# Performance work log

Measured on AMD Instinct MI355X. Metric: run time of the kernel, lower is better.

Reference implementation:

```python
import jax, jax.numpy as jnp
import numpy as np

EPS = 1e-6

def setup_inputs() -> dict:
    key = jax.random.key(0)
    k1, k2, k3, k4, k5 = jax.random.split(key, 5)
    B, Lq, Lk, D, Dc = 8, 1024, 8192, 256, 128
    q = jax.random.normal(k1, (B, Lq, D), dtype=jnp.float32)
    k_q = jax.random.randint(k2, (B, Lk, Dc), 0, 16, dtype=jnp.int32)  # 4-bit codes
    k_scale = jax.random.uniform(k3, (B, 1, Dc), dtype=jnp.float32)
    k_zero = jax.random.uniform(k4, (B, 1, Dc), dtype=jnp.float32) * 15.0
    W_up = jax.random.normal(k5, (D, Dc), dtype=jnp.float32) / np.sqrt(Dc)
    return {"q": q, "k_q": k_q, "k_scale": k_scale, "k_zero": k_zero, "W_up": W_up}

def reference(q, k_q, k_scale, k_zero, W_up):
    # int4 dequantization: (B, Lk, Dc)
    k_c = k_scale * (k_q.astype(jnp.float32) - k_zero)
    # low-rank decompress (nn.Linear(d_compressed, d_model, bias=False)): k = k_c @ W_up.T -> (B, Lk, D)
    k = jnp.einsum('blc,dc->bld', k_c, W_up)
    # squared norms (raw values used in diff, clamped values used in denominator)
    q_sq = jnp.sum(q * q, axis=-1)  # (B, Lq)
    k_sq = jnp.sum(k * k, axis=-1)  # (B, Lk)
    q_norm_sq = jnp.minimum(q_sq, 1.0 - EPS)
    k_norm_sq = jnp.minimum(k_sq, 1.0 - EPS)
    # ||q_i - k_j||^2 via expansion (same math as materializing the diff tensor)
    qk = jnp.einsum('bqd,bkd->bqk', q, k)  # (B, Lq, Lk)
    diff_norm_sq = jnp.maximum(q_sq[:, :, None] + k_sq[:, None, :] - 2.0 * qk, 0.0)
    denom = (1.0 - q_norm_sq)[:, :, None] * (1.0 - k_norm_sq)[:, None, :] + EPS
    dist = jnp.arccosh(1.0 + 2.0 * diff_norm_sq / denom)  # (B, Lq, Lk)
    return dist
```

## Files before the change

kernel.cpp:

```cpp
#include <hip/hip_runtime.h>
#include <hip/hip_bf16.h>

#define B_   8
#define LQ   1024
#define LK   8192
#define D_   256
#define DC   128
#define EPSF 1e-6f

typedef __attribute__((ext_vector_type(8))) short short8;
typedef __attribute__((ext_vector_type(4))) float floatx4;

static __device__ __forceinline__ floatx4 mfma16(short8 a, short8 b, floatx4 c) {
    return __builtin_amdgcn_mfma_f32_16x16x32_bf16(a, b, c, 0, 0, 0);
}
static __device__ __forceinline__ float fast_rcp(float x)  { return __builtin_amdgcn_rcpf(x); }
static __device__ __forceinline__ float fast_sqrt(float x) { return __builtin_amdgcn_sqrtf(x); }
static __device__ __forceinline__ float fast_ln(float x)   { return 0.69314718056f * __builtin_amdgcn_logf(x); }

static __device__ __forceinline__ void gl16(const void* g, void* l) {
    __builtin_amdgcn_global_load_lds(
        (const __attribute__((address_space(1))) unsigned int*)g,
        (__attribute__((address_space(3))) unsigned int*)l, 16, 0, 0);
}

__global__ __launch_bounds__(512) void k_G(const float* __restrict__ W,
                                           __hip_bfloat16* __restrict__ G,
                                           __hip_bfloat16* __restrict__ Wt) {
    __shared__ float red[512];
    int c1 = blockIdx.x;
    int t = threadIdx.x, c2 = t & 127, h = t >> 7;
    int d0 = h * 64;
    float a0 = 0.f, a1 = 0.f, a2 = 0.f, a3 = 0.f;
#pragma unroll 4
    for (int d = 0; d < 64; d += 4) {
        a0 += W[(size_t)(d0 + d + 0) * DC + c1] * W[(size_t)(d0 + d + 0) * DC + c2];
        a1 += W[(size_t)(d0 + d + 1) * DC + c1] * W[(size_t)(d0 + d + 1) * DC + c2];
        a2 += W[(size_t)(d0 + d + 2) * DC + c1] * W[(size_t)(d0 + d + 2) * DC + c2];
        a3 += W[(size_t)(d0 + d + 3) * DC + c1] * W[(size_t)(d0 + d + 3) * DC + c2];
    }
    red[t] = (a0 + a1) + (a2 + a3);
    if (t < 256) Wt[(size_t)c1 * D_ + t] = __float2bfloat16(W[(size_t)t * DC + c1]);
    __syncthreads();
    if (h == 0)
        G[c1 * DC + c2] =
            __float2bfloat16(red[c2] + red[128 + c2] + red[256 + c2] + red[384 + c2]);
}

__global__ __launch_bounds__(256) void k_qproj(const float* __restrict__ q,
                                               const __hip_bfloat16* __restrict__ Wt,
                                               __hip_bfloat16* __restrict__ qproj,
                                               float* __restrict__ q_sq) {
    __shared__ __hip_bfloat16 sA[32 * 72];
    __shared__ __hip_bfloat16 sB[128 * 72];
    int t = threadIdx.x, lane = t & 63, w = t >> 6;
    int quad = lane >> 4, li = lane & 15;
    int wm = w >> 1, wn = w & 1;
    int row0 = blockIdx.x * 32;

    float psum[2] = {0.f, 0.f};
    floatx4 acc[4];
#pragma unroll
    for (int nt = 0; nt < 4; ++nt) acc[nt] = (floatx4){0.f, 0.f, 0.f, 0.f};

    for (int kc4 = 0; kc4 < 4; ++kc4) {
#pragma unroll
        for (int it = 0; it < 2; ++it) {
            int idx = it * 256 + t;
            int r = idx >> 4, pos = idx & 15;
            float4 v = *(const float4*)(q + (size_t)(row0 + r) * D_ + kc4 * 64 + pos * 4);
            psum[it] += v.x * v.x + v.y * v.y + v.z * v.z + v.w * v.w;
            __hip_bfloat16* dst = &sA[r * 72 + pos * 4];
            dst[0] = __float2bfloat16(v.x); dst[1] = __float2bfloat16(v.y);
            dst[2] = __float2bfloat16(v.z); dst[3] = __float2bfloat16(v.w);
        }
#pragma unroll
        for (int it = 0; it < 4; ++it) {
            int e = it * 256 + t;
            int c = e >> 3, ch = e & 7;
            *(uint4*)&sB[c * 72 + ch * 8] =
                *(const uint4*)(Wt + (size_t)c * D_ + kc4 * 64 + ch * 8);
        }
        __syncthreads();
        short8 af[2];
#pragma unroll
        for (int ks = 0; ks < 2; ++ks)
            af[ks] = *(const short8*)&sA[(wm * 16 + li) * 72 + ks * 32 + quad * 8];
#pragma unroll
        for (int nt = 0; nt < 4; ++nt)
#pragma unroll
            for (int ks = 0; ks < 2; ++ks) {
                short8 bf = *(const short8*)&sB[((wn * 4 + nt) * 16 + li) * 72 + ks * 32 + quad * 8];
                acc[nt] = mfma16(af[ks], bf, acc[nt]);
            }
        __syncthreads();
    }
#pragma unroll
    for (int nt = 0; nt < 4; ++nt)
#pragma unroll
        for (int r = 0; r < 4; ++r) {
            int row = wm * 16 + quad * 4 + r;
            qproj[(size_t)(row0 + row) * DC + (wn * 4 + nt) * 16 + li] =
                __float2bfloat16(acc[nt][r]);
        }
#pragma unroll
    for (int it = 0; it < 2; ++it) {
        float s = psum[it];
        s += __shfl_xor(s, 1); s += __shfl_xor(s, 2);
        s += __shfl_xor(s, 4); s += __shfl_xor(s, 8);
        if (li == 0) q_sq[row0 + it * 16 + w * 4 + quad] = s;
    }
}

__global__ __launch_bounds__(256) void k_dq_ksq(const int* __restrict__ kq,
                                                const float* __restrict__ kscale,
                                                const float* __restrict__ kzero,
                                                const __hip_bfloat16* __restrict__ G,
                                                __hip_bfloat16* __restrict__ kc,
                                                float* __restrict__ k_sq) {
    __shared__ __hip_bfloat16 sK[64 * 132];
    int t = threadIdx.x, lane = t & 63, w = t >> 6;
    int quad = lane >> 4, li = lane & 15;
    int b = blockIdx.x >> 7, l0 = (blockIdx.x & 127) * 64;

    const int4* codes = (const int4*)(kq + ((size_t)b * LK + l0) * DC);
    int col = (t & 31) * 4;
    float4 sc = *(const float4*)(kscale + b * DC + col);
    float4 zp = *(const float4*)(kzero + b * DC + col);
    __hip_bfloat16* kco = kc + ((size_t)b * LK + l0) * DC;
#pragma unroll
    for (int it = 0; it < 8; ++it) {
        int idx = it * 256 + t;
        int r = idx >> 5;
        int4 c4 = codes[idx];
        __hip_bfloat16 tmp[4];
        tmp[0] = __float2bfloat16(sc.x * ((float)c4.x - zp.x));
        tmp[1] = __float2bfloat16(sc.y * ((float)c4.y - zp.y));
        tmp[2] = __float2bfloat16(sc.z * ((float)c4.z - zp.z));
        tmp[3] = __float2bfloat16(sc.w * ((float)c4.w - zp.w));
        *(uint2*)&sK[r * 132 + col] = *(const uint2*)tmp;
        *(uint2*)(kco + idx * 4)    = *(const uint2*)tmp;
    }
    __syncthreads();

    short8 af[4];
#pragma unroll
    for (int ks = 0; ks < 4; ++ks)
        af[ks] = *(const short8*)&sK[(w * 16 + li) * 132 + ks * 32 + quad * 8];
    float s4[4] = {0.f, 0.f, 0.f, 0.f};
#pragma unroll
    for (int nt = 0; nt < 8; ++nt) {
        floatx4 a0 = (floatx4){0.f, 0.f, 0.f, 0.f};
#pragma unroll
        for (int ks = 0; ks < 4; ++ks) {
            short8 bf = *(const short8*)(G + (size_t)(nt * 16 + li) * DC + ks * 32 + quad * 8);
            a0 = mfma16(af[ks], bf, a0);
        }
        int c2 = nt * 16 + li;
#pragma unroll
        for (int r = 0; r < 4; ++r)
            s4[r] += a0[r] * __bfloat162float(sK[(w * 16 + quad * 4 + r) * 132 + c2]);
    }
#pragma unroll
    for (int r = 0; r < 4; ++r) {
        float v = s4[r];
        v += __shfl_xor(v, 1); v += __shfl_xor(v, 2);
        v += __shfl_xor(v, 4); v += __shfl_xor(v, 8);
        if (li == 0)
            k_sq[(size_t)b * LK + l0 + w * 16 + quad * 4 + r] = v;
    }
}

__global__ __launch_bounds__(256, 4) void k_main(const __hip_bfloat16* __restrict__ qproj,
                                                 const __hip_bfloat16* __restrict__ kc,
                                                 const float* __restrict__ q_sq,
                                                 const float* __restrict__ k_sq,
                                                 float* __restrict__ out) {
    __shared__ __hip_bfloat16 sA[128 * 64];
    __shared__ __hip_bfloat16 sB[128 * 64];
    int t = threadIdx.x, lane = t & 63, w = t >> 6;
    int quad = lane >> 4, li = lane & 15;
    int wm = w >> 1, wn = w & 1;
    int bid = blockIdx.x;
    int b   = bid & 7;
    int rem = bid >> 3;
    int m0  = (rem & 7) << 7;
    int n0  = (rem >> 3) << 7;
    const char* Ag = (const char*)(qproj + ((size_t)b * LQ + m0) * DC);
    const char* Bg = (const char*)(kc   + ((size_t)b * LK + n0) * DC);

    int lrow = lane >> 3;
    int lch  = (lane & 7) ^ lrow;

    floatx4 acc[4][4];
#pragma unroll
    for (int i = 0; i < 4; ++i)
#pragma unroll
        for (int j = 0; j < 4; ++j)
            acc[i][j] = (floatx4){0.f, 0.f, 0.f, 0.f};

#pragma unroll
    for (int h = 0; h < 2; ++h) {
#pragma unroll
        for (int it = 0; it < 4; ++it) {
            int rbase = it * 32 + w * 8;
            size_t goff = (size_t)(rbase + lrow) * 256 + (size_t)(h * 8 + lch) * 16;
            gl16(Ag + goff, (char*)sA + rbase * 128);
            gl16(Bg + goff, (char*)sB + rbase * 128);
        }
        __syncthreads();
#pragma unroll
        for (int ks = 0; ks < 2; ++ks) {
            int ac = ((ks * 4 + quad) ^ (li & 7)) * 16;
            short8 qf[4], kf[4];
#pragma unroll
            for (int i = 0; i < 4; ++i) {
                qf[i] = *(const short8*)((const char*)sA + (wm * 64 + i * 16 + li) * 128 + ac);
                kf[i] = *(const short8*)((const char*)sB + (wn * 64 + i * 16 + li) * 128 + ac);
            }
#pragma unroll
            for (int i = 0; i < 4; ++i)
#pragma unroll
                for (int j = 0; j < 4; ++j)
                    acc[i][j] = mfma16(kf[j], qf[i], acc[i][j]);
        }
        if (h == 0) __syncthreads();
    }

    floatx4 ks4[4], kn4[4];
#pragma unroll
    for (int j = 0; j < 4; ++j) {
        ks4[j] = *(const floatx4*)(k_sq + (size_t)b * LK + n0 + wn * 64 + j * 16 + quad * 4);
#pragma unroll
        for (int r = 0; r < 4; ++r)
            kn4[j][r] = 1.f - fminf(ks4[j][r], 1.f - EPSF);
    }
#pragma unroll
    for (int i = 0; i < 4; ++i) {
        int m = m0 + wm * 64 + i * 16 + li;
        float qs  = q_sq[(size_t)b * LQ + m];
        float omq = 1.f - fminf(qs, 1.f - EPSF);
        float* orow = out + ((size_t)b * LQ + m) * (size_t)LK + n0 + wn * 64;
#pragma unroll
        for (int j = 0; j < 4; ++j) {
            floatx4 o;
#pragma unroll
            for (int r = 0; r < 4; ++r) {
                float diff  = fmaxf(qs + ks4[j][r] - 2.f * acc[i][j][r], 0.f);
                float delta = 2.f * diff * fast_rcp(omq * kn4[j][r] + EPSF);
                float sq    = fast_sqrt(delta * (delta + 2.f));
                o[r] = fast_ln(1.f + delta + sq);
            }
            __builtin_nontemporal_store(o, (floatx4*)(orow + j * 16 + quad * 4));
        }
    }
}

extern "C" void kernel_launch(void* const* d_in, const int* in_sizes, int n_in,
                              void* d_out, int out_size, void* d_ws, size_t ws_size,
                              hipStream_t stream) {
    const float* q      = (const float*)d_in[0];
    const int*   kq     = (const int*)d_in[1];
    const float* kscale = (const float*)d_in[2];
    const float* kzero  = (const float*)d_in[3];
    const float* W      = (const float*)d_in[4];
    float* out = (float*)d_out;

    char* ws = (char*)d_ws;
    __hip_bfloat16* qproj = (__hip_bfloat16*)(ws);
    __hip_bfloat16* kc    = (__hip_bfloat16*)(ws + 2097152);
    __hip_bfloat16* G     = (__hip_bfloat16*)(ws + 18874368);
    float*          q_sq  = (float*)(ws + 18907136);
    float*          k_sq  = (float*)(ws + 18939904);
    __hip_bfloat16* Wt    = kc;

    k_G     <<<128, 512, 0, stream>>>(W, G, Wt);
    k_qproj <<<256, 256, 0, stream>>>(q, Wt, qproj, q_sq);
    k_dq_ksq<<<1024, 256, 0, stream>>>(kq, kscale, kzero, G, kc, k_sq);
    k_main  <<<4096, 256, 0, stream>>>(qproj, kc, q_sq, k_sq, out);
}
```

Before: 357.1 us.

## Merge prep kernels, stage output through LDS for coalesced stores, persist main blocks

The q-projection and dequant/k_sq kernels are fused into one launch that branches on block index, and Wt is moved into the output buffer so it no longer aliases kc. The main kernel now loops over four N-tiles per block, 1024 blocks instead of 4096, reusing the A tile pointer and the q_sq values across tiles. Each accumulator half is written into LDS and read back so that threads store contiguous 64-float row segments, giving more coalesced nontemporal writes of the large output. The cost is extra LDS traffic and barriers, a larger shared allocation that may limit occupancy, and the A tile still being reloaded for every N-tile.

```diff
diff --git a/kernel.cpp b/kernel.cpp
--- a/kernel.cpp
+++ b/kernel.cpp
@@ -47,16 +47,16 @@
             __float2bfloat16(red[c2] + red[128 + c2] + red[256 + c2] + red[384 + c2]);
 }
 
-__global__ __launch_bounds__(256) void k_qproj(const float* __restrict__ q,
-                                               const __hip_bfloat16* __restrict__ Wt,
-                                               __hip_bfloat16* __restrict__ qproj,
-                                               float* __restrict__ q_sq) {
-    __shared__ __hip_bfloat16 sA[32 * 72];
-    __shared__ __hip_bfloat16 sB[128 * 72];
+static __device__ __forceinline__ void qproj_body(
+        char* smem, int blk,
+        const float* __restrict__ q, const __hip_bfloat16* __restrict__ Wt,
+        __hip_bfloat16* __restrict__ qproj, float* __restrict__ q_sq) {
+    __hip_bfloat16* sA = (__hip_bfloat16*)smem;
+    __hip_bfloat16* sB = sA + 32 * 72;
     int t = threadIdx.x, lane = t & 63, w = t >> 6;
     int quad = lane >> 4, li = lane & 15;
     int wm = w >> 1, wn = w & 1;
-    int row0 = blockIdx.x * 32;
+    int row0 = blk * 32;
 
     float psum[2] = {0.f, 0.f};
     floatx4 acc[4];
@@ -112,16 +112,15 @@
     }
 }
 
-__global__ __launch_bounds__(256) void k_dq_ksq(const int* __restrict__ kq,
-                                                const float* __restrict__ kscale,
-                                                const float* __restrict__ kzero,
-                                                const __hip_bfloat16* __restrict__ G,
-                                                __hip_bfloat16* __restrict__ kc,
-                                                float* __restrict__ k_sq) {
-    __shared__ __hip_bfloat16 sK[64 * 132];
+static __device__ __forceinline__ void dq_body(
+        char* smem, int blk,
+        const int* __restrict__ kq, const float* __restrict__ kscale,
+        const float* __restrict__ kzero, const __hip_bfloat16* __restrict__ G,
+        __hip_bfloat16* __restrict__ kc, float* __restrict__ k_sq) {
+    __hip_bfloat16* sK = (__hip_bfloat16*)smem;
     int t = threadIdx.x, lane = t & 63, w = t >> 6;
     int quad = lane >> 4, li = lane & 15;
-    int b = blockIdx.x >> 7, l0 = (blockIdx.x & 127) * 64;
+    int b = blk >> 7, l0 = (blk & 127) * 64;
 
     const int4* codes = (const int4*)(kq + ((size_t)b * LK + l0) * DC);
     int col = (t & 31) * 4;
@@ -171,87 +170,129 @@
     }
 }
 
+__global__ __launch_bounds__(256) void k_prep(const float* __restrict__ q,
+                                              const __hip_bfloat16* __restrict__ Wt,
+                                              __hip_bfloat16* __restrict__ qproj,
+                                              float* __restrict__ q_sq,
+                                              const int* __restrict__ kq,
+                                              const float* __restrict__ kscale,
+                                              const float* __restrict__ kzero,
+                                              const __hip_bfloat16* __restrict__ G,
+                                              __hip_bfloat16* __restrict__ kc,
+                                              float* __restrict__ k_sq) {
+    __shared__ __align__(16) char smem[23040];
+    if (blockIdx.x < 256)
+        qproj_body(smem, blockIdx.x, q, Wt, qproj, q_sq);
+    else
+        dq_body(smem, blockIdx.x - 256, kq, kscale, kzero, G, kc, k_sq);
+}
+
 __global__ __launch_bounds__(256, 4) void k_main(const __hip_bfloat16* __restrict__ qproj,
                                                  const __hip_bfloat16* __restrict__ kc,
                                                  const float* __restrict__ q_sq,
                                                  const float* __restrict__ k_sq,
                                                  float* __restrict__ out) {
-    __shared__ __hip_bfloat16 sA[128 * 64];
-    __shared__ __hip_bfloat16 sB[128 * 64];
+    __shared__ __align__(16) char smem[34816];
+    __hip_bfloat16* sA = (__hip_bfloat16*)smem;
+    __hip_bfloat16* sB = sA + 128 * 64;
+    float* sO = (float*)smem;
+
     int t = threadIdx.x, lane = t & 63, w = t >> 6;
     int quad = lane >> 4, li = lane & 15;
     int wm = w >> 1, wn = w & 1;
-    int bid = blockIdx.x;
-    int b   = bid & 7;
-    int rem = bid >> 3;
-    int m0  = (rem & 7) << 7;
-    int n0  = (rem >> 3) << 7;
+    int blk = blockIdx.x;
+    int b    = blk & 7;
+    int rem0 = blk >> 3;
+    int m0   = (rem0 & 7) << 7;
+    int nt0  = rem0 >> 3;
     const char* Ag = (const char*)(qproj + ((size_t)b * LQ + m0) * DC);
-    const char* Bg = (const char*)(kc   + ((size_t)b * LK + n0) * DC);
 
     int lrow = lane >> 3;
     int lch  = (lane & 7) ^ lrow;
 
-    floatx4 acc[4][4];
-#pragma unroll
-    for (int i = 0; i < 4; ++i)
-#pragma unroll
-        for (int j = 0; j < 4; ++j)
-            acc[i][j] = (floatx4){0.f, 0.f, 0.f, 0.f};
-
-#pragma unroll
-    for (int h = 0; h < 2; ++h) {
-#pragma unroll
-        for (int it = 0; it < 4; ++it) {
-            int rbase = it * 32 + w * 8;
-            size_t goff = (size_t)(rbase + lrow) * 256 + (size_t)(h * 8 + lch) * 16;
-            gl16(Ag + goff, (char*)sA + rbase * 128);
-            gl16(Bg + goff, (char*)sB + rbase * 128);
-        }
-        __syncthreads();
-#pragma unroll
-        for (int ks = 0; ks < 2; ++ks) {
-            int ac = ((ks * 4 + quad) ^ (li & 7)) * 16;
-            short8 qf[4], kf[4];
-#pragma unroll
-            for (int i = 0; i < 4; ++i) {
-                qf[i] = *(const short8*)((const char*)sA + (wm * 64 + i * 16 + li) * 128 + ac);
-                kf[i] = *(const short8*)((const char*)sB + (wn * 64 + i * 16 + li) * 128 + ac);
-            }
-#pragma unroll
-            for (int i = 0; i < 4; ++i)
-#pragma unroll
-                for (int j = 0; j < 4; ++j)
-                    acc[i][j] = mfma16(kf[j], qf[i], acc[i][j]);
-        }
-        if (h == 0) __syncthreads();
-    }
-
-    floatx4 ks4[4], kn4[4];
-#pragma unroll
-    for (int j = 0; j < 4; ++j) {
-        ks4[j] = *(const floatx4*)(k_sq + (size_t)b * LK + n0 + wn * 64 + j * 16 + quad * 4);
-#pragma unroll
-        for (int r = 0; r < 4; ++r)
-            kn4[j][r] = 1.f - fminf(ks4[j][r], 1.f - EPSF);
-    }
-#pragma unroll
-    for (int i = 0; i < 4; ++i) {
-        int m = m0 + wm * 64 + i * 16 + li;
-        float qs  = q_sq[(size_t)b * LQ + m];
-        float omq = 1.f - fminf(qs, 1.f - EPSF);
-        float* orow = out + ((size_t)b * LQ + m) * (size_t)LK + n0 + wn * 64;
-#pragma unroll
-        for (int j = 0; j < 4; ++j) {
-            floatx4 o;
-#pragma unroll
-            for (int r = 0; r < 4; ++r) {
-                float diff  = fmaxf(qs + ks4[j][r] - 2.f * acc[i][j][r], 0.f);
-                float delta = 2.f * diff * fast_rcp(omq * kn4[j][r] + EPSF);
-                float sq    = fast_sqrt(delta * (delta + 2.f));
-                o[r] = fast_ln(1.f + delta + sq);
-            }
-            __builtin_nontemporal_store(o, (floatx4*)(orow + j * 16 + quad * 4));
+    int orow_t = t >> 4;
+    int ocol4  = (t & 15) * 4;
+    float qsA[8], omqA[8];
+#pragma unroll
+    for (int qq = 0; qq < 8; ++qq) {
+        qsA[qq]  = q_sq[(size_t)b * LQ + m0 + qq * 16 + orow_t];
+        omqA[qq] = 1.f - fminf(qsA[qq], 1.f - EPSF);
+    }
+
+    for (int s = 0; s < 4; ++s) {
+        int n0 = (nt0 + s * 16) << 7;
+        const char* Bg = (const char*)(kc + ((size_t)b * LK + n0) * DC);
+
+        floatx4 acc[4][4];
+#pragma unroll
+        for (int i = 0; i < 4; ++i)
+#pragma unroll
+            for (int j = 0; j < 4; ++j)
+                acc[i][j] = (floatx4){0.f, 0.f, 0.f, 0.f};
+
+#pragma unroll
+        for (int h = 0; h < 2; ++h) {
+#pragma unroll
+            for (int it = 0; it < 4; ++it) {
+                int rbase = it * 32 + w * 8;
+                size_t goff = (size_t)(rbase + lrow) * 256 + (size_t)(h * 8 + lch) * 16;
+                gl16(Ag + goff, (char*)sA + rbase * 128);
+                gl16(Bg + goff, (char*)sB + rbase * 128);
+            }
+            __syncthreads();
+#pragma unroll
+            for (int ks = 0; ks < 2; ++ks) {
+                int ac = ((ks * 4 + quad) ^ (li & 7)) * 16;
+                short8 qf[4], kf[4];
+#pragma unroll
+                for (int i = 0; i < 4; ++i) {
+                    qf[i] = *(const short8*)((const char*)sA + (wm * 64 + i * 16 + li) * 128 + ac);
+                    kf[i] = *(const short8*)((const char*)sB + (wn * 64 + i * 16 + li) * 128 + ac);
+                }
+#pragma unroll
+                for (int i = 0; i < 4; ++i)
+#pragma unroll
+                    for (int j = 0; j < 4; ++j)
+                        acc[i][j] = mfma16(kf[j], qf[i], acc[i][j]);
+            }
+            __syncthreads();
+        }
+
+#pragma unroll
+        for (int p = 0; p < 2; ++p) {
+#pragma unroll
+            for (int jj = 0; jj < 2; ++jj) {
+                int c = wn * 32 + jj * 16 + quad * 4;
+#pragma unroll
+                for (int i = 0; i < 4; ++i) {
+                    int m = wm * 64 + i * 16 + li;
+                    *(floatx4*)&sO[m * 68 + c] = acc[i][p * 2 + jj];
+                }
+            }
+            __syncthreads();
+            int nbase = (ocol4 >> 5) * 64 + p * 32 + (ocol4 & 31);
+            floatx4 ks4 = *(const floatx4*)(k_sq + (size_t)b * LK + n0 + nbase);
+            floatx4 kn;
+#pragma unroll
+            for (int r = 0; r < 4; ++r)
+                kn[r] = 1.f - fminf(ks4[r], 1.f - EPSF);
+#pragma unroll
+            for (int qq = 0; qq < 8; ++qq) {
+                int row = qq * 16 + orow_t;
+                floatx4 v = *(const floatx4*)&sO[row * 68 + ocol4];
+                float qs = qsA[qq], omq = omqA[qq];
+                floatx4 o;
+#pragma unroll
+                for (int r = 0; r < 4; ++r) {
+                    float diff  = fmaxf(qs + ks4[r] - 2.f * v[r], 0.f);
+                    float delta = 2.f * diff * fast_rcp(omq * kn[r] + EPSF);
+                    float sq    = fast_sqrt(delta * (delta + 2.f));
+                    o[r] = fast_ln(1.f + delta + sq);
+                }
+                __builtin_nontemporal_store(
+                    o, (floatx4*)(out + ((size_t)b * LQ + m0 + row) * (size_t)LK + n0 + nbase));
+            }
+            __syncthreads();
         }
     }
 }
@@ -272,10 +313,9 @@
     __hip_bfloat16* G     = (__hip_bfloat16*)(ws + 18874368);
     float*          q_sq  = (float*)(ws + 18907136);
     float*          k_sq  = (float*)(ws + 18939904);
-    __hip_bfloat16* Wt    = kc;
-
-    k_G     <<<128, 512, 0, stream>>>(W, G, Wt);
-    k_qproj <<<256, 256, 0, stream>>>(q, Wt, qproj, q_sq);
-    k_dq_ksq<<<1024, 256, 0, stream>>>(kq, kscale, kzero, G, kc, k_sq);
-    k_main  <<<4096, 256, 0, stream>>>(qproj, kc, q_sq, k_sq, out);
-}
+    __hip_bfloat16* Wt    = (__hip_bfloat16*)out;
+
+    k_G    <<<128, 512, 0, stream>>>(W, G, Wt);
+    k_prep <<<1280, 256, 0, stream>>>(q, Wt, qproj, q_sq, kq, kscale, kzero, G, kc, k_sq);
+    k_main <<<1024, 256, 0, stream>>>(qproj, kc, q_sq, k_sq, out);
+}
```

Result: no change. 361.3 us (+1.2%).
